# Optimization experiments

Hardware: AMD Instinct MI355X
Metric: run time of the kernel (lower is better)

The kernel has to match this reference:

```python
import jax, jax.numpy as jnp
import numpy as np
from jax import lax

NB, C, HEADS, DH, MULT = 3, 64, 4, 16, 4  # num_blocks, dim, heads, dim_head, ffn mult

def _dw(x, k):
    # depthwise conv, NHWC, kernel HWIO with I=1, O=C, SAME padding
    return lax.conv_general_dilated(x, k, (1, 1), 'SAME',
                                    dimension_numbers=('NHWC', 'HWIO', 'NHWC'),
                                    feature_group_count=x.shape[-1])

def _l2n(t, eps=1e-6):
    # torch F.normalize(p=2, eps): x / max(||x||, eps) over last dim
    n = jnp.sqrt(jnp.sum(t * t, -1, keepdims=True))
    return t / jnp.maximum(n, eps)

def _ln(x, g, b, eps=1e-5):
    mu = jnp.mean(x, -1, keepdims=True)
    var = jnp.mean((x - mu) ** 2, -1, keepdims=True)
    return (x - mu) / jnp.sqrt(var + eps) * g + b

def _msa(x, m, Wq, Wk, Wv, resc, Wp, bp, pe1, pe2, w1, b1, w2, b2, dwk, db):
    # x, m: [b,h,w,c] (NHWC)
    b, h, w, c = x.shape
    n = h * w
    xf = x.reshape(b, n, c)
    q = xf @ Wq
    k = xf @ Wk
    v = xf @ Wv
    # mask-guided mechanism (1x1 convs == channel matmuls, 5x5 depthwise)
    m1 = m @ w1 + b1
    am = jax.nn.sigmoid(_dw(m1 @ w2 + b2, dwk) + db)
    ma = (m1 * am + m1).reshape(b, n, c)
    vg = v * ma  # mask gating of V (elementwise, head split commutes)
    hd = lambda t: t.reshape(b, n, HEADS, DH).transpose(0, 2, 3, 1)  # b,H,d,n
    qh = _l2n(hd(q))
    kh = _l2n(hd(k))
    vh = hd(vg)
    # transposed (channel) attention: [d,n]x[n,d] -> [d,d]
    attn = jnp.einsum('bhdn,bhen->bhde', kh, qh) * resc[None, :, None, None]
    attn = jax.nn.softmax(attn, -1)
    o = jnp.einsum('bhde,bhen->bhdn', attn, vh).transpose(0, 3, 1, 2).reshape(b, n, c)
    out_c = (o @ Wp + bp).reshape(b, h, w, c)
    # positional embedding on ungated v_inp: dwconv3 -> GELU -> dwconv3
    vi = v.reshape(b, h, w, c)
    out_p = _dw(jax.nn.gelu(_dw(vi, pe1), approximate=False), pe2)
    return out_c + out_p

def _ff(x, w1, dwk, w2):
    h1 = jax.nn.gelu(x @ w1, approximate=False)          # 1x1 conv expand
    h2 = jax.nn.gelu(_dw(h1, dwk), approximate=False)     # 3x3 depthwise
    return h2 @ w2                                        # 1x1 conv project

def setup_inputs() -> dict:
    key = jax.random.key(0)
    ks = iter(jax.random.split(key, 24))
    r = lambda sh, s=0.02: jax.random.normal(next(ks), sh, jnp.float32) * s
    B, H, W = 2, 256, 256
    return {
        'x': jax.random.normal(next(ks), (B, C, H, W), jnp.float32),
        'mask': jax.random.normal(next(ks), (B, C, H, W), jnp.float32),
        'Wq': r((NB, C, C)), 'Wk': r((NB, C, C)), 'Wv': r((NB, C, C)),
        'rescale': jnp.ones((NB, HEADS), jnp.float32),
        'Wp': r((NB, C, C)), 'bp': jnp.zeros((NB, C), jnp.float32),
        'pe1': r((NB, 3, 3, 1, C)), 'pe2': r((NB, 3, 3, 1, C)),
        'mm_w1': r((NB, C, C)), 'mm_b1': jnp.zeros((NB, C), jnp.float32),
        'mm_w2': r((NB, C, C)), 'mm_b2': jnp.zeros((NB, C), jnp.float32),
        'mm_dw': r((NB, 5, 5, 1, C)), 'mm_db': jnp.zeros((NB, C), jnp.float32),
        'ln_g': jnp.ones((NB, C), jnp.float32), 'ln_b': jnp.zeros((NB, C), jnp.float32),
        'ff_w1': r((NB, C, C * MULT)), 'ff_dw': r((NB, 3, 3, 1, C * MULT)),
        'ff_w2': r((NB, C * MULT, C)),
    }

def reference(x, mask, Wq, Wk, Wv, rescale, Wp, bp, pe1, pe2, mm_w1, mm_b1,
              mm_w2, mm_b2, mm_dw, mm_db, ln_g, ln_b, ff_w1, ff_dw, ff_w2):
    xh = x.transpose(0, 2, 3, 1)     # NCHW -> NHWC
    mh = mask.transpose(0, 2, 3, 1)
    for i in range(NB):
        xh = _msa(xh, mh, Wq[i], Wk[i], Wv[i], rescale[i], Wp[i], bp[i],
                  pe1[i], pe2[i], mm_w1[i], mm_b1[i], mm_w2[i], mm_b2[i],
                  mm_dw[i], mm_db[i]) + xh
        xh = _ff(_ln(xh, ln_g[i], ln_b[i]), ff_w1[i], ff_dw[i], ff_w2[i]) + xh
    return xh.transpose(0, 3, 1, 2)  # NHWC -> NCHW
```

## Files before the change

kernel.cpp:

```cpp
#include <hip/hip_runtime.h>
#include <math.h>


typedef unsigned short bhalf;
typedef unsigned int u32;
typedef _Float16 h2 __attribute__((ext_vector_type(2)));
typedef _Float16 f16x4 __attribute__((ext_vector_type(4)));
typedef _Float16 f16x8 __attribute__((ext_vector_type(8)));
typedef __attribute__((ext_vector_type(4))) float f32x4;

#define GEMM_GRID 2048
#define NSPLIT 32
#define SCOPY 2304
#define WBLK 57344

__device__ __forceinline__ float h2f(bhalf b) {
  union { bhalf u; _Float16 h; } c; c.u = b; return (float)c.h;
}
__device__ __forceinline__ bhalf f2h(float f) {
  union { _Float16 h; bhalf u; } c; c.h = (_Float16)f; return c.u;
}
__device__ __forceinline__ u32 pack2h(float a, float b) {
  auto r = __builtin_amdgcn_cvt_pkrtz(a, b);
  union { decltype(r) h; u32 u; } c; c.h = r; return c.u;
}
__device__ __forceinline__ void unpack2h(u32 p, float& a, float& b) {
  union { u32 u; h2 h; } c; c.u = p;
  a = (float)c.h[0]; b = (float)c.h[1];
}
__device__ __forceinline__ void unpack8h(uint4 u, float* f) {
  unpack2h(u.x, f[0], f[1]); unpack2h(u.y, f[2], f[3]);
  unpack2h(u.z, f[4], f[5]); unpack2h(u.w, f[6], f[7]);
}
__device__ __forceinline__ float gelu_f(float v) {
  return 0.5f * v * (1.0f + erff(v * 0.70710678118654752440f));
}
__device__ __forceinline__ uint4 pack16(const float* v) {
  uint4 s;
  s.x = pack2h(v[0], v[1]); s.y = pack2h(v[2], v[3]);
  s.z = pack2h(v[4], v[5]); s.w = pack2h(v[6], v[7]);
  return s;
}
__device__ __forceinline__ f16x4 cvt4h(f32x4 v) {
  union { u32 u[2]; f16x4 h; } c;
  c.u[0] = pack2h(v[0], v[1]); c.u[1] = pack2h(v[2], v[3]);
  return c.h;
}

__global__ __launch_bounds__(256) void prep_weights(
    const float* __restrict__ mm_w1, const float* __restrict__ mm_w2,
    const float* __restrict__ Wq, const float* __restrict__ Wk,
    const float* __restrict__ Wv, const float* __restrict__ Wp,
    const float* __restrict__ ff_w1, const float* __restrict__ ff_w2,
    bhalf* __restrict__ out)
{
  int i = blockIdx.x >> 3, slot = blockIdx.x & 7;
  int t = threadIdx.x;
  const float* src; int ksh, N; size_t off;
  switch (slot) {
    case 0:  src = mm_w1 + i*4096;  ksh=6; N=64;  off = 0;     break;
    case 1:  src = mm_w2 + i*4096;  ksh=6; N=64;  off = 4096;  break;
    case 2:  src = Wq + i*4096;     ksh=6; N=64;  off = 8192;  break;
    case 3:  src = Wk + i*4096;     ksh=6; N=64;  off = 12288; break;
    case 4:  src = Wv + i*4096;     ksh=6; N=64;  off = 16384; break;
    case 5:  src = Wp + i*4096;     ksh=6; N=64;  off = 20480; break;
    case 6:  src = ff_w1 + i*16384; ksh=6; N=256; off = 24576; break;
    default: src = ff_w2 + i*16384; ksh=8; N=64;  off = 40960; break;
  }
  bhalf* dst = out + (size_t)i * WBLK + off;
  int sz = N << ksh;
  int kmask = (1 << ksh) - 1;
  for (int idx = t; idx < sz; idx += 256) {
    int n = idx >> ksh, k = idx & kmask;
    dst[idx] = f2h(src[k * N + n]);
  }
}

template<int MODE>
__global__ __launch_bounds__(256) void nchw2nhwc(const float* __restrict__ in,
                                                 void* __restrict__ out,
                                                 bhalf* __restrict__ out2) {
  __shared__ float tile[64][65];
  int t = threadIdx.x;
  int b = blockIdx.x >> 10;
  int n0 = (blockIdx.x & 1023) << 6;
  #pragma unroll
  for (int j = 0; j < 16; ++j) {
    int idx = j * 256 + t;
    int c = idx >> 6, nn = idx & 63;
    tile[c][nn] = in[(((size_t)(b * 64 + c)) << 16) + n0 + nn];
  }
  __syncthreads();
  #pragma unroll
  for (int j = 0; j < 16; ++j) {
    int idx = j * 256 + t;
    int nn = idx >> 6, c = idx & 63;
    size_t o = ((((size_t)b << 16) + n0 + nn) << 6) + c;
    float v = tile[c][nn];
    if (MODE == 0) { ((float*)out)[o] = v; out2[o] = f2h(v); }
    else           { ((bhalf*)out)[o] = f2h(v); }
  }
}

__global__ __launch_bounds__(256) void nhwc2nchw(const float* __restrict__ in,
                                                 float* __restrict__ out) {
  __shared__ float tile[64][65];
  int t = threadIdx.x;
  int b = blockIdx.x >> 10;
  int n0 = (blockIdx.x & 1023) << 6;
  #pragma unroll
  for (int j = 0; j < 16; ++j) {
    int idx = j * 256 + t;
    int nn = idx >> 6, c = idx & 63;
    tile[c][nn] = in[((((size_t)b << 16) + n0 + nn) << 6) + c];
  }
  __syncthreads();
  #pragma unroll
  for (int j = 0; j < 16; ++j) {
    int idx = j * 256 + t;
    int c = idx >> 6, nn = idx & 63;
    out[(((size_t)(b * 64 + c)) << 16) + n0 + nn] = tile[c][nn];
  }
}

__global__ __launch_bounds__(256) void gemm_mask2(
    const bhalf* __restrict__ M, const bhalf* __restrict__ wt,
    const float* __restrict__ b1, const float* __restrict__ b2,
    bhalf* __restrict__ T1o, bhalf* __restrict__ T2o)
{
  __shared__ __align__(16) char smem[9216 * 2 + 17408];
  bhalf* WT1 = (bhalf*)smem;
  bhalf* WT2 = (bhalf*)(smem + 9216);
  float* Cs  = (float*)(smem + 18432);
  bhalf* Ab  = (bhalf*)(smem + 18432);
  __shared__ float b1s[64], b2s[64];
  int t = threadIdx.x;
  {
    const uint4* ws = (const uint4*)wt;
    #pragma unroll
    for (int i = 0; i < 4; ++i) {
      int idx4 = i * 256 + t;
      int n = (idx4 >> 3) & 63, q4 = idx4 & 7;
      uint4* wd = (idx4 < 512) ? (uint4*)WT1 : (uint4*)WT2;
      wd[n * 9 + q4] = ws[idx4];
    }
    if (t < 64) { b1s[t] = b1[t]; b2s[t] = b2[t]; }
  }
  __syncthreads();

  int wv = t >> 6, lane = t & 63;
  int lm = lane & 15, q = lane >> 4;
  size_t row0 = ((size_t)blockIdx.x << 6) + (wv << 4);
  int rr = t >> 2, c0 = (t & 3) << 4;
  size_t grow = ((size_t)blockIdx.x << 6) + rr;

  const bhalf* arow = M + ((row0 + lm) << 6) + (q << 3);
  f16x8 a0 = *(const f16x8*)(arow);
  f16x8 a1 = *(const f16x8*)(arow + 32);
  f32x4 acc[4];
  #pragma unroll
  for (int nt = 0; nt < 4; ++nt) {
    const bhalf* bp_ = &WT1[(nt * 16 + lm) * 72 + (q << 3)];
    f16x8 bv0 = *(const f16x8*)(bp_);
    f16x8 bv1 = *(const f16x8*)(bp_ + 32);
    f32x4 c = {0.f, 0.f, 0.f, 0.f};
    c = __builtin_amdgcn_mfma_f32_16x16x32_f16(a0, bv0, c, 0, 0, 0);
    c = __builtin_amdgcn_mfma_f32_16x16x32_f16(a1, bv1, c, 0, 0, 0);
    acc[nt] = c;
  }
  #pragma unroll
  for (int nt = 0; nt < 4; ++nt)
    #pragma unroll
    for (int r = 0; r < 4; ++r)
      Cs[((wv << 4) + (q << 2) + r) * 68 + (nt << 4) + lm] = acc[nt][r];
  __syncthreads();
  float v[16];
  #pragma unroll
  for (int j = 0; j < 4; ++j) {
    float4 u = *(const float4*)&Cs[rr * 68 + c0 + 4 * j];
    v[4*j] = u.x; v[4*j+1] = u.y; v[4*j+2] = u.z; v[4*j+3] = u.w;
  }
  #pragma unroll
  for (int j = 0; j < 16; ++j) v[j] += b1s[c0 + j];
  uint4 p0 = pack16(v), p1 = pack16(v + 8);
  bhalf* ob1 = T1o + (grow << 6) + c0;
  ((uint4*)ob1)[0] = p0; ((uint4*)ob1)[1] = p1;
  __syncthreads();
  *(uint4*)&Ab[rr * 72 + c0]     = p0;
  *(uint4*)&Ab[rr * 72 + c0 + 8] = p1;
  __syncthreads();

  const bhalf* ar2 = &Ab[((wv << 4) + lm) * 72 + (q << 3)];
  f16x8 c0v = *(const f16x8*)(ar2);
  f16x8 c1v = *(const f16x8*)(ar2 + 32);
  #pragma unroll
  for (int nt = 0; nt < 4; ++nt) {
    const bhalf* bp_ = &WT2[(nt * 16 + lm) * 72 + (q << 3)];
    f16x8 bv0 = *(const f16x8*)(bp_);
    f16x8 bv1 = *(const f16x8*)(bp_ + 32);
    f32x4 c = {0.f, 0.f, 0.f, 0.f};
    c = __builtin_amdgcn_mfma_f32_16x16x32_f16(c0v, bv0, c, 0, 0, 0);
    c = __builtin_amdgcn_mfma_f32_16x16x32_f16(c1v, bv1, c, 0, 0, 0);
    acc[nt] = c;
  }
  __syncthreads();
  #pragma unroll
  for (int nt = 0; nt < 4; ++nt)
    #pragma unroll
    for (int r = 0; r < 4; ++r)
      Cs[((wv << 4) + (q << 2) + r) * 68 + (nt << 4) + lm] = acc[nt][r];
  __syncthreads();
  #pragma unroll
  for (int j = 0; j < 4; ++j) {
    float4 u = *(const float4*)&Cs[rr * 68 + c0 + 4 * j];
    v[4*j] = u.x; v[4*j+1] = u.y; v[4*j+2] = u.z; v[4*j+3] = u.w;
  }
  #pragma unroll
  for (int j = 0; j < 16; ++j) v[j] += b2s[c0 + j];
  bhalf* ob2 = T2o + (grow << 6) + c0;
  ((uint4*)ob2)[0] = pack16(v);
  ((uint4*)ob2)[1] = pack16(v + 8);
}

#define EP_BIAS 1
#define EP_RESID 5

template<int EP, int BW>
__global__ __launch_bounds__(256) void gemm64m(
    const bhalf* __restrict__ in_, const bhalf* __restrict__ wt,
    const float* __restrict__ bias, void* __restrict__ out_,
    const bhalf* __restrict__ aux, bhalf* __restrict__ xbout)
{
  __shared__ __align__(16) char smem[64 * 68 * 4];
  bhalf* WT = (bhalf*)smem;
  float* Cs = (float*)smem;
  __shared__ float bias_s[64];
  int t = threadIdx.x;
  if (BW) wt += (size_t)(blockIdx.x >> 10) << 12;
  {
    const uint4* ws = (const uint4*)wt;
    uint4* wd = (uint4*)WT;
    #pragma unroll
    for (int i = 0; i < 2; ++i) {
      int idx4 = i * 256 + t;
      int n = idx4 >> 3, q4 = idx4 & 7;
      wd[n * 9 + q4] = ws[idx4];
    }
    if (t < 64) bias_s[t] = bias[t];
  }
  __syncthreads();

  int wv = t >> 6, lane = t & 63;
  int lm = lane & 15, q = lane >> 4;
  size_t row0 = ((size_t)blockIdx.x << 6) + (wv << 4);

  const bhalf* arow = in_ + ((row0 + lm) << 6) + (q << 3);
  f16x8 a0 = *(const f16x8*)(arow);
  f16x8 a1 = *(const f16x8*)(arow + 32);

  f32x4 acc[4];
  #pragma unroll
  for (int nt = 0; nt < 4; ++nt) {
    const bhalf* bp_ = &WT[(nt * 16 + lm) * 72 + (q << 3)];
    f16x8 b0 = *(const f16x8*)(bp_);
    f16x8 b1 = *(const f16x8*)(bp_ + 32);
    f32x4 c = {0.f, 0.f, 0.f, 0.f};
    c = __builtin_amdgcn_mfma_f32_16x16x32_f16(a0, b0, c, 0, 0, 0);
    c = __builtin_amdgcn_mfma_f32_16x16x32_f16(a1, b1, c, 0, 0, 0);
    acc[nt] = c;
  }
  __syncthreads();
  #pragma unroll
  for (int nt = 0; nt < 4; ++nt)
    #pragma unroll
    for (int r = 0; r < 4; ++r)
      Cs[((wv << 4) + (q << 2) + r) * 68 + (nt << 4) + lm] = acc[nt][r];
  __syncthreads();

  int rr = t >> 2, c0 = (t & 3) << 4;
  size_t grow = ((size_t)blockIdx.x << 6) + rr;
  float v[16];
  #pragma unroll
  for (int j = 0; j < 4; ++j) {
    float4 u = *(const float4*)&Cs[rr * 68 + c0 + 4 * j];
    v[4*j] = u.x; v[4*j+1] = u.y; v[4*j+2] = u.z; v[4*j+3] = u.w;
  }

  if (EP == EP_RESID) {
    float* xr = (float*)out_ + (grow << 6) + c0;
    const bhalf* pr = aux + (grow << 6) + c0;
    uint4 p0 = ((const uint4*)pr)[0], p1 = ((const uint4*)pr)[1];
    float pf[16];
    unpack8h(p0, pf); unpack8h(p1, pf + 8);
    #pragma unroll
    for (int j = 0; j < 4; ++j) {
      float4* x4 = (float4*)(xr + 4 * j);
      float4 u = *x4;
      u.x += v[4*j]   + bias_s[c0 + 4*j]     + pf[4*j];
      u.y += v[4*j+1] + bias_s[c0 + 4*j + 1] + pf[4*j+1];
      u.z += v[4*j+2] + bias_s[c0 + 4*j + 2] + pf[4*j+2];
      u.w += v[4*j+3] + bias_s[c0 + 4*j + 3] + pf[4*j+3];
      *x4 = u;
      v[4*j] = u.x; v[4*j+1] = u.y; v[4*j+2] = u.z; v[4*j+3] = u.w;
    }
    bhalf* xb = xbout + (grow << 6) + c0;
    ((uint4*)xb)[0] = pack16(v);
    ((uint4*)xb)[1] = pack16(v + 8);
  } else {
    #pragma unroll
    for (int j = 0; j < 16; ++j) v[j] += bias_s[c0 + j];
    bhalf* ob = (bhalf*)out_ + (grow << 6) + c0;
    ((uint4*)ob)[0] = pack16(v);
    ((uint4*)ob)[1] = pack16(v + 8);
  }
}

__global__ __launch_bounds__(256) void qkv_gemm(
    const bhalf* __restrict__ xb, const bhalf* __restrict__ wt,
    const bhalf* __restrict__ ma, bhalf* __restrict__ Vb,
    bhalf* __restrict__ VG, float* __restrict__ S)
{
  __shared__ __align__(16) char smem[27648];
  bhalf* WT = (bhalf*)smem;
  float* Cs = (float*)smem;
  float* Sred = (float*)smem;
  float* qred = (float*)(smem + 16384);
  float* kred = (float*)(smem + 17408);
  int t = threadIdx.x;
  {
    const uint4* ws = (const uint4*)wt;
    uint4* wd = (uint4*)WT;
    #pragma unroll
    for (int i = 0; i < 6; ++i) {
      int idx4 = i * 256 + t;
      int n = idx4 >> 3, q4 = idx4 & 7;
      wd[n * 9 + q4] = ws[idx4];
    }
  }
  __syncthreads();

  int wv_ = t >> 6, lane = t & 63;
  int lm = lane & 15, q = lane >> 4;
  int rr = t >> 2, c0 = (t & 3) << 4;

  f32x4 accS[4];
  f32x4 accV[2][4];
  float qss[4] = {0.f, 0.f, 0.f, 0.f};
  float kss[4] = {0.f, 0.f, 0.f, 0.f};
  #pragma unroll
  for (int h = 0; h < 4; ++h) accS[h] = (f32x4){0.f, 0.f, 0.f, 0.f};

  #pragma unroll
  for (int grp = 0; grp < 2; ++grp) {
    size_t row0 = ((size_t)blockIdx.x << 7) + (grp << 6) + (wv_ << 4);
    const bhalf* arow = xb + ((row0 + lm) << 6) + (q << 3);
    f16x8 a0 = *(const f16x8*)(arow);
    f16x8 a1 = *(const f16x8*)(arow + 32);
    f32x4 accQ[4], accK[4];
    #pragma unroll
    for (int nt = 0; nt < 4; ++nt) {
      const bhalf* bp_ = &WT[(nt * 16 + lm) * 72 + (q << 3)];
      f32x4 c = {0.f, 0.f, 0.f, 0.f};
      c = __builtin_amdgcn_mfma_f32_16x16x32_f16(a0, *(const f16x8*)(bp_), c, 0, 0, 0);
      c = __builtin_amdgcn_mfma_f32_16x16x32_f16(a1, *(const f16x8*)(bp_ + 32), c, 0, 0, 0);
      accQ[nt] = c;
    }
    #pragma unroll
    for (int nt = 0; nt < 4; ++nt) {
      const bhalf* bp_ = &WT[((64 + nt * 16) + lm) * 72 + (q << 3)];
      f32x4 c = {0.f, 0.f, 0.f, 0.f};
      c = __builtin_amdgcn_mfma_f32_16x16x32_f16(a0, *(const f16x8*)(bp_), c, 0, 0, 0);
      c = __builtin_amdgcn_mfma_f32_16x16x32_f16(a1, *(const f16x8*)(bp_ + 32), c, 0, 0, 0);
      accK[nt] = c;
    }
    #pragma unroll
    for (int nt = 0; nt < 4; ++nt) {
      const bhalf* bp_ = &WT[((128 + nt * 16) + lm) * 72 + (q << 3)];
      f32x4 c = {0.f, 0.f, 0.f, 0.f};
      c = __builtin_amdgcn_mfma_f32_16x16x32_f16(a0, *(const f16x8*)(bp_), c, 0, 0, 0);
      c = __builtin_amdgcn_mfma_f32_16x16x32_f16(a1, *(const f16x8*)(bp_ + 32), c, 0, 0, 0);
      accV[grp][nt] = c;
    }
    #pragma unroll
    for (int h = 0; h < 4; ++h) {
      f16x4 kf = cvt4h(accK[h]);
      f16x4 qf = cvt4h(accQ[h]);
      accS[h] = __builtin_amdgcn_mfma_f32_16x16x16f16(kf, qf, accS[h], 0, 0, 0);
      #pragma unroll
      for (int r = 0; r < 4; ++r) {
        qss[h] += accQ[h][r] * accQ[h][r];
        kss[h] += accK[h][r] * accK[h][r];
      }
    }
  }

  #pragma unroll
  for (int grp = 0; grp < 2; ++grp) {
    __syncthreads();
    #pragma unroll
    for (int nt = 0; nt < 4; ++nt)
      #pragma unroll
      for (int r = 0; r < 4; ++r)
        Cs[((wv_ << 4) + (q << 2) + r) * 68 + (nt << 4) + lm] = accV[grp][nt][r];
    __syncthreads();
    float v[16];
    #pragma unroll
    for (int j = 0; j < 4; ++j) {
      float4 u = *(const float4*)&Cs[rr * 68 + c0 + 4 * j];
      v[4*j] = u.x; v[4*j+1] = u.y; v[4*j+2] = u.z; v[4*j+3] = u.w;
    }
    size_t grow = ((size_t)blockIdx.x << 7) + (grp << 6) + rr;
    bhalf* ob = Vb + (grow << 6) + c0;
    ((uint4*)ob)[0] = pack16(v);
    ((uint4*)ob)[1] = pack16(v + 8);
    const bhalf* mr = ma + (grow << 6) + c0;
    uint4 m0 = ((const uint4*)mr)[0], m1q = ((const uint4*)mr)[1];
    float mf[16];
    unpack8h(m0, mf); unpack8h(m1q, mf + 8);
    float gv[16];
    #pragma unroll
    for (int j = 0; j < 16; ++j) gv[j] = v[j] * mf[j];
    bhalf* gb = VG + (grow << 6) + c0;
    ((uint4*)gb)[0] = pack16(gv);
    ((uint4*)gb)[1] = pack16(gv + 8);
  }
  __syncthreads();

  #pragma unroll
  for (int h = 0; h < 4; ++h)
    #pragma unroll
    for (int r = 0; r < 4; ++r)
      Sred[(wv_ << 10) + (h << 8) + ((q << 2) + r) * 16 + lm] = accS[h][r];
  #pragma unroll
  for (int nt = 0; nt < 4; ++nt) {
    qss[nt] += __shfl_xor(qss[nt], 16); qss[nt] += __shfl_xor(qss[nt], 32);
    kss[nt] += __shfl_xor(kss[nt], 16); kss[nt] += __shfl_xor(kss[nt], 32);
  }
  if (q == 0) {
    #pragma unroll
    for (int nt = 0; nt < 4; ++nt) {
      qred[(wv_ << 6) + (nt << 4) + lm] = qss[nt];
      kred[(wv_ << 6) + (nt << 4) + lm] = kss[nt];
    }
  }
  __syncthreads();

  int b = (int)(blockIdx.x >> 9);
  float* Sc = S + (size_t)(blockIdx.x & (NSPLIT - 1)) * SCOPY;
  {
    int ci = t << 2;
    float4 s = {0.f, 0.f, 0.f, 0.f};
    #pragma unroll
    for (int wv2 = 0; wv2 < 4; ++wv2) {
      float4 u = *(const float4*)&Sred[(wv2 << 10) + ci];
      s.x += u.x; s.y += u.y; s.z += u.z; s.w += u.w;
    }
    float* sp = Sc + b * 1024 + ci;
    atomicAdd(sp + 0, s.x); atomicAdd(sp + 1, s.y);
    atomicAdd(sp + 2, s.z); atomicAdd(sp + 3, s.w);
  }
  if (t < 64) {
    float qs = qred[t] + qred[64 + t] + qred[128 + t] + qred[192 + t];
    float ks = kred[t] + kred[64 + t] + kred[128 + t] + kred[192 + t];
    atomicAdd(Sc + 2048 + b * 64 + t, qs);
    atomicAdd(Sc + 2176 + b * 64 + t, ks);
  }
}

__global__ __launch_bounds__(256) void ffn_gemm1_ln(
    const float* __restrict__ X, const bhalf* __restrict__ wt,
    const float* __restrict__ g, const float* __restrict__ bb,
    bhalf* __restrict__ out_)
{
  __shared__ __align__(16) char smem[256 * 72 * 2];
  bhalf* WT = (bhalf*)smem;
  float* Cs = (float*)smem;
  __shared__ float gs[64], bs[64];
  int t = threadIdx.x;
  {
    const uint4* ws = (const uint4*)wt;
    uint4* wd = (uint4*)WT;
    #pragma unroll
    for (int i = 0; i < 8; ++i) {
      int idx4 = i * 256 + t;
      int n = idx4 >> 3, q4 = idx4 & 7;
      wd[n * 9 + q4] = ws[idx4];
    }
    if (t < 64) { gs[t] = g[t]; bs[t] = bb[t]; }
  }
  __syncthreads();

  int wv_ = t >> 6, lane = t & 63;
  int lm = lane & 15, q = lane >> 4;
  size_t row0 = ((size_t)blockIdx.x << 6) + (wv_ << 4);
  const float* xr = X + ((row0 + lm) << 6);
  int k0 = q << 3;
  float xa[8], xb2[8];
  {
    float4 u0 = *(const float4*)(xr + k0);
    float4 u1 = *(const float4*)(xr + k0 + 4);
    float4 u2 = *(const float4*)(xr + 32 + k0);
    float4 u3 = *(const float4*)(xr + 32 + k0 + 4);
    xa[0]=u0.x; xa[1]=u0.y; xa[2]=u0.z; xa[3]=u0.w;
    xa[4]=u1.x; xa[5]=u1.y; xa[6]=u1.z; xa[7]=u1.w;
    xb2[0]=u2.x; xb2[1]=u2.y; xb2[2]=u2.z; xb2[3]=u2.w;
    xb2[4]=u3.x; xb2[5]=u3.y; xb2[6]=u3.z; xb2[7]=u3.w;
  }
  float s1 = 0.f, s2 = 0.f;
  #pragma unroll
  for (int j = 0; j < 8; ++j) {
    s1 += xa[j] + xb2[j];
    s2 += xa[j] * xa[j] + xb2[j] * xb2[j];
  }
  s1 += __shfl_xor(s1, 16); s1 += __shfl_xor(s1, 32);
  s2 += __shfl_xor(s2, 16); s2 += __shfl_xor(s2, 32);
  float mu = s1 * 0.015625f;
  float var = s2 * 0.015625f - mu * mu;
  float rstd = rsqrtf(var + 1e-5f);
  f16x8 a0, a1;
  #pragma unroll
  for (int j = 0; j < 8; ++j) {
    a0[j] = (_Float16)((xa[j]  - mu) * rstd * gs[k0 + j]      + bs[k0 + j]);
    a1[j] = (_Float16)((xb2[j] - mu) * rstd * gs[32 + k0 + j] + bs[32 + k0 + j]);
  }

  f32x4 acc[16];
  #pragma unroll
  for (int nt = 0; nt < 16; ++nt) {
    const bhalf* bp_ = &WT[(nt * 16 + lm) * 72 + (q << 3)];
    f16x8 b0 = *(const f16x8*)(bp_);
    f16x8 b1 = *(const f16x8*)(bp_ + 32);
    f32x4 c = {0.f, 0.f, 0.f, 0.f};
    c = __builtin_amdgcn_mfma_f32_16x16x32_f16(a0, b0, c, 0, 0, 0);
    c = __builtin_amdgcn_mfma_f32_16x16x32_f16(a1, b1, c, 0, 0, 0);
    acc[nt] = c;
  }

  int rr = t >> 2, c0 = (t & 3) << 4;
  size_t grow = ((size_t)blockIdx.x << 6) + rr;
  #pragma unroll
  for (int gi = 0; gi < 4; ++gi) {
    __syncthreads();
    #pragma unroll
    for (int nt = 0; nt < 4; ++nt)
      #pragma unroll
      for (int r = 0; r < 4; ++r)
        Cs[((wv_ << 4) + (q << 2) + r) * 68 + (nt << 4) + lm] = acc[gi * 4 + nt][r];
    __syncthreads();
    float v[16];
    #pragma unroll
    for (int j = 0; j < 4; ++j) {
      float4 u = *(const float4*)&Cs[rr * 68 + c0 + 4 * j];
      v[4*j]   = gelu_f(u.x); v[4*j+1] = gelu_f(u.y);
      v[4*j+2] = gelu_f(u.z); v[4*j+3] = gelu_f(u.w);
    }
    bhalf* ob = out_ + (grow << 8) + (gi << 6) + c0;
    ((uint4*)ob)[0] = pack16(v);
    ((uint4*)ob)[1] = pack16(v + 8);
  }
}

__global__ __launch_bounds__(256) void ffn_gemm2(
    const bhalf* __restrict__ in_, const bhalf* __restrict__ wt,
    float* __restrict__ X, bhalf* __restrict__ Xb)
{
  __shared__ __align__(16) char smem[64 * 264 * 2];
  bhalf* WT = (bhalf*)smem;
  float* Cs = (float*)smem;
  int t = threadIdx.x;
  {
    const uint4* ws = (const uint4*)wt;
    uint4* wd = (uint4*)WT;
    #pragma unroll
    for (int i = 0; i < 8; ++i) {
      int idx4 = i * 256 + t;
      int n = idx4 >> 5, q4 = idx4 & 31;
      wd[n * 33 + q4] = ws[idx4];
    }
  }
  __syncthreads();

  int wv_ = t >> 6, lane = t & 63;
  int lm = lane & 15, q = lane >> 4;
  size_t row0 = ((size_t)blockIdx.x << 6) + (wv_ << 4);
  const bhalf* arow = in_ + ((row0 + lm) << 8) + (q << 3);
  f16x8 a[8];
  #pragma unroll
  for (int ch = 0; ch < 8; ++ch) a[ch] = *(const f16x8*)(arow + 32 * ch);

  f32x4 acc[4];
  #pragma unroll
  for (int nt = 0; nt < 4; ++nt) {
    const bhalf* bp_ = &WT[(nt * 16 + lm) * 264 + (q << 3)];
    f32x4 c = {0.f, 0.f, 0.f, 0.f};
    #pragma unroll
    for (int ch = 0; ch < 8; ++ch) {
      f16x8 b = *(const f16x8*)(bp_ + 32 * ch);
      c = __builtin_amdgcn_mfma_f32_16x16x32_f16(a[ch], b, c, 0, 0, 0);
    }
    acc[nt] = c;
  }
  __syncthreads();
  #pragma unroll
  for (int nt = 0; nt < 4; ++nt)
    #pragma unroll
    for (int r = 0; r < 4; ++r)
      Cs[((wv_ << 4) + (q << 2) + r) * 68 + (nt << 4) + lm] = acc[nt][r];
  __syncthreads();

  int rr = t >> 2, c0 = (t & 3) << 4;
  size_t grow = ((size_t)blockIdx.x << 6) + rr;
  float v[16];
  #pragma unroll
  for (int j = 0; j < 4; ++j) {
    float4 u = *(const float4*)&Cs[rr * 68 + c0 + 4 * j];
    v[4*j] = u.x; v[4*j+1] = u.y; v[4*j+2] = u.z; v[4*j+3] = u.w;
  }
  float* xr = X + (grow << 6) + c0;
  #pragma unroll
  for (int j = 0; j < 4; ++j) {
    float4* x4 = (float4*)(xr + 4 * j);
    float4 u = *x4;
    u.x += v[4*j]; u.y += v[4*j+1]; u.z += v[4*j+2]; u.w += v[4*j+3];
    *x4 = u;
    v[4*j] = u.x; v[4*j+1] = u.y; v[4*j+2] = u.z; v[4*j+3] = u.w;
  }
  bhalf* xb = Xb + (grow << 6) + c0;
  ((uint4*)xb)[0] = pack16(v);
  ((uint4*)xb)[1] = pack16(v + 8);
}

template<int KS, int EPI, int CH>
__global__ __launch_bounds__(256) void dwconv4(
    const bhalf* __restrict__ in, const float* __restrict__ wt,
    const float* __restrict__ db, const bhalf* __restrict__ m1,
    bhalf* __restrict__ out, int wstride)
{
  const int CB = (CH == 64) ? 6 : 8;
  const int G  = CH >> 3;
  const int GB = (CH == 64) ? 3 : 5;
  const int R  = KS >> 1;
  const int NCOL = KS + 3;
  __shared__ u32 Wsu[KS * KS * G * 5];
  __shared__ float db_s[64];
  int t = threadIdx.x;
  for (int idx = t; idx < KS * KS * (CH >> 1); idx += 256) {
    int tap = idx >> (CB - 1), cp = idx & ((CH >> 1) - 1);
    int cg = cp >> 2, j = cp & 3;
    h2 p;
    p[0] = (_Float16)wt[tap * wstride + 2 * cp];
    p[1] = (_Float16)wt[tap * wstride + 2 * cp + 1];
    union { h2 h; u32 u; } cv; cv.h = p;
    Wsu[tap * (G * 5) + cg * 5 + j] = cv.u;
  }
  if (EPI == 2 && t < 64) db_s[t] = db[t];
  __syncthreads();

  size_t gid = (size_t)blockIdx.x * 256 + t;
  int cg = (int)gid & (G - 1);
  int c0 = cg << 3;
  size_t p4 = gid >> GB;
  int x0 = ((int)(p4 & 63)) << 2;
  int hy = (int)((p4 >> 6) & 255);
  size_t bb = p4 >> 14;

  h2 zero = {(_Float16)0.0f, (_Float16)0.0f};
  h2 acc[4][4];
  #pragma unroll
  for (int o = 0; o < 4; ++o)
    #pragma unroll
    for (int j = 0; j < 4; ++j) acc[o][j] = zero;

  #pragma unroll
  for (int kh = 0; kh < KS; ++kh) {
    int y = hy + kh - R;
    if ((unsigned)y >= 256u) continue;
    h2 wr[KS][4];
    #pragma unroll
    for (int kw = 0; kw < KS; ++kw) {
      const u32* wp = &Wsu[(kh * KS + kw) * (G * 5) + cg * 5];
      #pragma unroll
      for (int j = 0; j < 4; ++j) {
        union { u32 u; h2 h; } cv; cv.u = wp[j]; wr[kw][j] = cv.h;
      }
    }
    const bhalf* rowp = in + (((((size_t)bb << 8) + (size_t)y) << 8) << CB) + c0;
    #pragma unroll
    for (int cc = 0; cc < NCOL; ++cc) {
      int xw = x0 + cc - R;
      if (cc < R || cc >= NCOL - R) {
        if ((unsigned)xw >= 256u) continue;
      }
      union { uint4 u; h2 h[4]; } dv;
      dv.u = *(const uint4*)(rowp + ((size_t)xw << CB));
      #pragma unroll
      for (int kw = 0; kw < KS; ++kw) {
        int o = cc - kw;
        if (o >= 0 && o < 4) {
          #pragma unroll
          for (int j = 0; j < 4; ++j)
            acc[o][j] += dv.h[j] * wr[kw][j];
        }
      }
    }
  }

  size_t p0 = ((((size_t)bb << 8) + (size_t)hy) << 8) + (size_t)x0;
  #pragma unroll
  for (int o = 0; o < 4; ++o) {
    bhalf* op = out + ((p0 + o) << CB) + c0;
    if (EPI == 0) {
      union { h2 h[4]; uint4 u; } sv;
      #pragma unroll
      for (int j = 0; j < 4; ++j) sv.h[j] = acc[o][j];
      *(uint4*)op = sv.u;
    } else if (EPI == 1) {
      float r[8];
      #pragma unroll
      for (int j = 0; j < 4; ++j) {
        r[2*j]   = gelu_f((float)acc[o][j][0]);
        r[2*j+1] = gelu_f((float)acc[o][j][1]);
      }
      *(uint4*)op = pack16(r);
    } else {
      uint4 mu = *(const uint4*)(m1 + ((p0 + o) << CB) + c0);
      float mf[8];
      unpack8h(mu, mf);
      float r[8];
      #pragma unroll
      for (int j = 0; j < 8; ++j) {
        float av = (float)acc[o][j >> 1][j & 1];
        float am = 1.0f / (1.0f + expf(-(av + db_s[c0 + j])));
        r[j] = mf[j] * (am + 1.0f);
      }
      *(uint4*)op = pack16(r);
    }
  }
}

__global__ __launch_bounds__(256) void attn_fold(
    const float* __restrict__ S, const float* __restrict__ resc,
    const bhalf* __restrict__ wpT, bhalf* __restrict__ weffT)
{
  __shared__ float As[1024];
  __shared__ float nqs_s[64];
  int b = blockIdx.x;
  int t = threadIdx.x;
  if (t < 64) {
    int h = t >> 4, d = t & 15;
    float nqsum = 0.f;
    for (int c = 0; c < NSPLIT; ++c)
      nqsum += S[c * SCOPY + 2048 + b * 64 + h * 16 + d];
    nqs_s[t] = fmaxf(sqrtf(nqsum), 1e-6f);
  }
  __syncthreads();
  if (t < 64) {
    int h = t >> 4, d = t & 15;
    float nksum = 0.f;
    for (int c = 0; c < NSPLIT; ++c)
      nksum += S[c * SCOPY + 2176 + b * 64 + h * 16 + d];
    float nkd = fmaxf(sqrtf(nksum), 1e-6f);
    float r = resc[h];
    float4 s4[4] = {{0,0,0,0},{0,0,0,0},{0,0,0,0},{0,0,0,0}};
    for (int c = 0; c < NSPLIT; ++c) {
      const float4* sp = (const float4*)&S[c * SCOPY + (((b * 4 + h) * 16 + d) << 4)];
      #pragma unroll
      for (int j = 0; j < 4; ++j) {
        float4 u = sp[j];
        s4[j].x += u.x; s4[j].y += u.y; s4[j].z += u.z; s4[j].w += u.w;
      }
    }
    float a[16];
    #pragma unroll
    for (int j = 0; j < 4; ++j) {
      a[4*j]   = s4[j].x * r / (nkd * nqs_s[h * 16 + 4*j]);
      a[4*j+1] = s4[j].y * r / (nkd * nqs_s[h * 16 + 4*j + 1]);
      a[4*j+2] = s4[j].z * r / (nkd * nqs_s[h * 16 + 4*j + 2]);
      a[4*j+3] = s4[j].w * r / (nkd * nqs_s[h * 16 + 4*j + 3]);
    }
    float m = -1e30f;
    #pragma unroll
    for (int e = 0; e < 16; ++e) m = fmaxf(m, a[e]);
    float sum = 0.f;
    #pragma unroll
    for (int e = 0; e < 16; ++e) { a[e] = expf(a[e] - m); sum += a[e]; }
    float inv = 1.0f / sum;
    #pragma unroll
    for (int e = 0; e < 16; ++e)
      As[((h * 16 + e) << 4) + d] = a[e] * inv;
  }
  __syncthreads();
  int m = t & 63, h = t >> 6;
  const bhalf* wp = wpT + m * 64 + h * 16;
  float wv_[16];
  uint4 w0 = ((const uint4*)wp)[0], w1 = ((const uint4*)wp)[1];
  unpack8h(w0, wv_); unpack8h(w1, wv_ + 8);
  float r2[16];
  #pragma unroll
  for (int e = 0; e < 16; ++e) {
    const float* ar = &As[(h * 16 + e) << 4];
    float s = 0.f;
    #pragma unroll
    for (int d = 0; d < 16; ++d) s += ar[d] * wv_[d];
    r2[e] = s;
  }
  bhalf* dst = weffT + b * 4096 + m * 64 + h * 16;
  ((uint4*)dst)[0] = pack16(r2);
  ((uint4*)dst)[1] = pack16(r2 + 8);
}

extern "C" void kernel_launch(void* const* d_in, const int* in_sizes, int n_in,
                              void* d_out, int out_size, void* d_ws, size_t ws_size,
                              hipStream_t stream)
{
  (void)in_sizes; (void)n_in; (void)out_size; (void)ws_size;
  const float* x_in    = (const float*)d_in[0];
  const float* mask_in = (const float*)d_in[1];
  const float* Wq    = (const float*)d_in[2];
  const float* Wk    = (const float*)d_in[3];
  const float* Wv    = (const float*)d_in[4];
  const float* resc  = (const float*)d_in[5];
  const float* Wp    = (const float*)d_in[6];
  const float* bp    = (const float*)d_in[7];
  const float* pe1   = (const float*)d_in[8];
  const float* pe2   = (const float*)d_in[9];
  const float* mm_w1 = (const float*)d_in[10];
  const float* mm_b1 = (const float*)d_in[11];
  const float* mm_w2 = (const float*)d_in[12];
  const float* mm_b2 = (const float*)d_in[13];
  const float* mm_dw = (const float*)d_in[14];
  const float* mm_db = (const float*)d_in[15];
  const float* ln_g  = (const float*)d_in[16];
  const float* ln_b  = (const float*)d_in[17];
  const float* ff_w1 = (const float*)d_in[18];
  const float* ff_dw = (const float*)d_in[19];
  const float* ff_w2 = (const float*)d_in[20];

  const size_t NC = 8388608;
  char* w = (char*)d_ws;
  float* X  = (float*)w; w += NC * 4;
  bhalf* Xb = (bhalf*)w; w += NC * 2;
  bhalf* M  = (bhalf*)w; w += NC * 2;
  bhalf* Qb = (bhalf*)w; w += NC * 2;
  bhalf* Kb = (bhalf*)w; w += NC * 2;
  bhalf* Vb = (bhalf*)w; w += NC * 2;
  bhalf* VG = (bhalf*)w; w += NC * 2;
  bhalf* T1 = (bhalf*)w; w += NC * 2;
  bhalf* T2 = (bhalf*)w; w += NC * 2;
  bhalf* T3 = (bhalf*)w; w += NC * 2;
  bhalf* Pb = (bhalf*)w; w += NC * 2;
  float* Sb    = (float*)w; w += (size_t)NSPLIT * SCOPY * 4;
  bhalf* WeffT = (bhalf*)w; w += 8192 * 2;
  bhalf* WTg   = (bhalf*)w; w += (size_t)3 * WBLK * 2;
  (void)Qb; (void)Kb;
  bhalf* F1 = Qb;
  bhalf* F2 = T1;

  prep_weights<<<24, 256, 0, stream>>>(mm_w1, mm_w2, Wq, Wk, Wv, Wp, ff_w1, ff_w2, WTg);
  nchw2nhwc<0><<<2048, 256, 0, stream>>>(x_in, X, Xb);
  nchw2nhwc<1><<<2048, 256, 0, stream>>>(mask_in, M, nullptr);

  for (int i = 0; i < 3; ++i) {
    const bhalf* wb = WTg + (size_t)i * WBLK;
    gemm_mask2<<<GEMM_GRID, 256, 0, stream>>>(M, wb + 0, mm_b1 + i*64, mm_b2 + i*64, T1, T2);
    dwconv4<5, 2, 64><<<1024, 256, 0, stream>>>(T2, mm_dw + i*1600, mm_db + i*64, T1, T3, 64);
    hipMemsetAsync(Sb, 0, NSPLIT * SCOPY * 4, stream);
    qkv_gemm<<<1024, 256, 0, stream>>>(Xb, wb + 8192, T3, Vb, VG, Sb);
    attn_fold<<<2, 256, 0, stream>>>(Sb, resc + i*4, wb + 20480, WeffT);
    dwconv4<3, 1, 64><<<1024, 256, 0, stream>>>(Vb, pe1 + i*576, nullptr, nullptr, T1, 64);
    dwconv4<3, 0, 64><<<1024, 256, 0, stream>>>(T1, pe2 + i*576, nullptr, nullptr, Pb, 64);
    gemm64m<EP_RESID, 1><<<GEMM_GRID, 256, 0, stream>>>(VG, WeffT, bp + i*64, X, Pb, Xb);
    ffn_gemm1_ln<<<GEMM_GRID, 256, 0, stream>>>(X, wb + 24576, ln_g + i*64, ln_b + i*64, F1);
    dwconv4<3, 1, 256><<<4096, 256, 0, stream>>>(F1, ff_dw + i*2304, nullptr, nullptr, F2, 256);
    ffn_gemm2<<<GEMM_GRID, 256, 0, stream>>>(F2, wb + 40960, X, Xb);
  }
  nhwc2nchw<<<2048, 256, 0, stream>>>(X, (float*)d_out);
}
```

Measured before the change: 839.8 us.

## Fuse final NCHW transpose into last FFN GEMM and use fast GELU/sigmoid

The last block's ffn_gemm2 now writes its result straight to the NCHW output through a shared-memory transpose. This removes the separate nhwc2nchw kernel along with the fp32 X writeback and its reread. Exact erf GELU is replaced by a tanh approximation built from __expf and rcp, and the sigmoid switches to fast exp and reciprocal. Both cut transcendental cost in the dwconv and GEMM epilogues, but they change numerics slightly (tanh GELU differs from exact GELU).

```diff
diff --git a/kernel.cpp b/kernel.cpp
--- a/kernel.cpp
+++ b/kernel.cpp
@@ -33,7 +33,10 @@
   unpack2h(u.z, f[4], f[5]); unpack2h(u.w, f[6], f[7]);
 }
 __device__ __forceinline__ float gelu_f(float v) {
-  return 0.5f * v * (1.0f + erff(v * 0.70710678118654752440f));
+  float u = v * (0.7978845608f + 0.03567740814f * v * v);
+  float e = __expf(2.0f * u);
+  float th = 1.0f - 2.0f * __builtin_amdgcn_rcpf(e + 1.0f);
+  return 0.5f * v * (1.0f + th);
 }
 __device__ __forceinline__ uint4 pack16(const float* v) {
   uint4 s;
@@ -102,27 +105,6 @@
   }
 }
 
-__global__ __launch_bounds__(256) void nhwc2nchw(const float* __restrict__ in,
-                                                 float* __restrict__ out) {
-  __shared__ float tile[64][65];
-  int t = threadIdx.x;
-  int b = blockIdx.x >> 10;
-  int n0 = (blockIdx.x & 1023) << 6;
-  #pragma unroll
-  for (int j = 0; j < 16; ++j) {
-    int idx = j * 256 + t;
-    int nn = idx >> 6, c = idx & 63;
-    tile[c][nn] = in[((((size_t)b << 16) + n0 + nn) << 6) + c];
-  }
-  __syncthreads();
-  #pragma unroll
-  for (int j = 0; j < 16; ++j) {
-    int idx = j * 256 + t;
-    int c = idx >> 6, nn = idx & 63;
-    out[(((size_t)(b * 64 + c)) << 16) + n0 + nn] = tile[c][nn];
-  }
-}
-
 __global__ __launch_bounds__(256) void gemm_mask2(
     const bhalf* __restrict__ M, const bhalf* __restrict__ wt,
     const float* __restrict__ b1, const float* __restrict__ b2,
@@ -560,9 +542,10 @@
   }
 }
 
+template<int FINAL>
 __global__ __launch_bounds__(256) void ffn_gemm2(
     const bhalf* __restrict__ in_, const bhalf* __restrict__ wt,
-    float* __restrict__ X, bhalf* __restrict__ Xb)
+    float* __restrict__ X, bhalf* __restrict__ Xb, float* __restrict__ out)
 {
   __shared__ __align__(16) char smem[64 * 264 * 2];
   bhalf* WT = (bhalf*)smem;
@@ -622,12 +605,28 @@
     float4* x4 = (float4*)(xr + 4 * j);
     float4 u = *x4;
     u.x += v[4*j]; u.y += v[4*j+1]; u.z += v[4*j+2]; u.w += v[4*j+3];
-    *x4 = u;
+    if (FINAL == 0) *x4 = u;
     v[4*j] = u.x; v[4*j+1] = u.y; v[4*j+2] = u.z; v[4*j+3] = u.w;
   }
-  bhalf* xb = Xb + (grow << 6) + c0;
-  ((uint4*)xb)[0] = pack16(v);
-  ((uint4*)xb)[1] = pack16(v + 8);
+  if (FINAL == 0) {
+    bhalf* xb = Xb + (grow << 6) + c0;
+    ((uint4*)xb)[0] = pack16(v);
+    ((uint4*)xb)[1] = pack16(v + 8);
+  } else {
+    __syncthreads();
+    #pragma unroll
+    for (int j = 0; j < 16; ++j)
+      Cs[(c0 + j) * 68 + rr] = v[j];
+    __syncthreads();
+    int bb2 = (int)(blockIdx.x >> 10);
+    int n0 = ((int)blockIdx.x & 1023) << 6;
+    #pragma unroll
+    for (int j = 0; j < 16; ++j) {
+      int idx = j * 256 + t;
+      int c = idx >> 6, nn = idx & 63;
+      out[(((size_t)(bb2 * 64 + c)) << 16) + n0 + nn] = Cs[c * 68 + nn];
+    }
+  }
 }
 
 template<int KS, int EPI, int CH>
@@ -730,7 +729,7 @@
       #pragma unroll
       for (int j = 0; j < 8; ++j) {
         float av = (float)acc[o][j >> 1][j & 1];
-        float am = 1.0f / (1.0f + expf(-(av + db_s[c0 + j])));
+        float am = __builtin_amdgcn_rcpf(1.0f + __expf(-(av + db_s[c0 + j])));
         r[j] = mf[j] * (am + 1.0f);
       }
       *(uint4*)op = pack16(r);
@@ -872,7 +871,9 @@
     gemm64m<EP_RESID, 1><<<GEMM_GRID, 256, 0, stream>>>(VG, WeffT, bp + i*64, X, Pb, Xb);
     ffn_gemm1_ln<<<GEMM_GRID, 256, 0, stream>>>(X, wb + 24576, ln_g + i*64, ln_b + i*64, F1);
     dwconv4<3, 1, 256><<<4096, 256, 0, stream>>>(F1, ff_dw + i*2304, nullptr, nullptr, F2, 256);
-    ffn_gemm2<<<GEMM_GRID, 256, 0, stream>>>(F2, wb + 40960, X, Xb);
-  }
-  nhwc2nchw<<<2048, 256, 0, stream>>>(X, (float*)d_out);
-}
+    if (i < 2)
+      ffn_gemm2<0><<<GEMM_GRID, 256, 0, stream>>>(F2, wb + 40960, X, Xb, nullptr);
+    else
+      ffn_gemm2<1><<<GEMM_GRID, 256, 0, stream>>>(F2, wb + 40960, X, Xb, (float*)d_out);
+  }
+}
```

After: 799.6 us. 1.05x faster.
